# Performance work log

Measured on AMD Instinct MI355X. Metric: run time of the kernel, lower is better.

The kernel has to match this reference:

```python
import jax, jax.numpy as jnp
import numpy as np

B, DEC, ENC, H = 4, 128, 512, 768


def setup_inputs() -> dict:
    key = jax.random.key(0)
    k1, k2, k3, k4, k5 = jax.random.split(key, 5)
    scale = 1.0 / np.sqrt(H)
    return {
        "decoder_state": jax.random.normal(k1, (B, DEC, H), dtype=jnp.float32),
        "encoder_outputs": jax.random.normal(k2, (B, ENC, H), dtype=jnp.float32),
        "mask": jnp.zeros((B, DEC, ENC), dtype=jnp.float32),
        # Learned params: torch nn.Linear(H, H, bias=False) weights, stored as (in, out)
        "W1": jax.random.normal(k3, (H, H), dtype=jnp.float32) * scale,
        "W2": jax.random.normal(k4, (H, H), dtype=jnp.float32) * scale,
        "vt": jax.random.normal(k5, (H,), dtype=jnp.float32) * scale,
    }


def reference(decoder_state, encoder_outputs, mask, W1, W2, vt):
    # enc_t: (B, enc, H), dec_t: (B, dec, H)
    enc_t = jnp.einsum("beh,hk->bek", encoder_outputs, W1)
    dec_t = jnp.einsum("bdh,hk->bdk", decoder_state, W2)
    # Bahdanau additive score: tanh of broadcast sum -> (B, dec, enc, H), reduce with vt
    hidden = jnp.tanh(enc_t[:, None, :, :] + dec_t[:, :, None, :])
    log_score = jnp.einsum("bdek,k->bde", hidden, vt)
    log_score_masked = log_score + mask
    return (log_score_masked, log_score)
```

## Files before the change

### kernel.cpp

```cpp
#include <hip/hip_runtime.h>
#include <hip/hip_bf16.h>

#define B_SZ   4
#define DEC_SZ 128
#define ENC_SZ 512
#define H_SZ   768
#define OUT_N  (B_SZ * DEC_SZ * ENC_SZ)

typedef __attribute__((ext_vector_type(8))) short s8v;
typedef __attribute__((ext_vector_type(4))) float fvec4;

__device__ inline unsigned short f2bf(float x) {
  union { float f; unsigned u; } v; v.f = x;
  unsigned r = v.u + 0x7FFF + ((v.u >> 16) & 1);
  return (unsigned short)(r >> 16);
}

__device__ inline s8v load8(const unsigned short* p) { return *(const s8v*)p; }
__device__ inline s8v load8(const float* p) {
  float4 a = ((const float4*)p)[0];
  float4 b = ((const float4*)p)[1];
  unsigned short r[8] = {f2bf(a.x), f2bf(a.y), f2bf(a.z), f2bf(a.w),
                         f2bf(b.x), f2bf(b.y), f2bf(b.z), f2bf(b.w)};
  return *(const s8v*)r;
}

__global__ __launch_bounds__(256) void transpose_w(const float* __restrict__ W1,
                                                   const float* __restrict__ W2,
                                                   unsigned short* __restrict__ T1,
                                                   unsigned short* __restrict__ T2) {
  const float* W = blockIdx.z ? W2 : W1;
  unsigned short* T = blockIdx.z ? T2 : T1;
  __shared__ float tile[64][65];
  int c0 = blockIdx.x * 64;
  int r0 = blockIdx.y * 64;
  int tx = threadIdx.x & 63, ty = threadIdx.x >> 6;
#pragma unroll
  for (int i = 0; i < 16; ++i) {
    int r = ty + i * 4;
    tile[r][tx] = W[(size_t)(r0 + r) * H_SZ + c0 + tx];
  }
  __syncthreads();
#pragma unroll
  for (int i = 0; i < 16; ++i) {
    int c = ty + i * 4;
    T[(size_t)(c0 + c) * H_SZ + r0 + tx] = f2bf(tile[tx][c]);
  }
}

template <bool TILED, typename TA, typename TB>
__device__ inline void gemm_body(const TA* __restrict__ A, const TB* __restrict__ B,
                                 float* __restrict__ C, int ldc, int bx, int by) {
  const int m0 = bx * 128;
  const int n0 = by * 64;

  __shared__ unsigned short As[128][40];
  __shared__ unsigned short Bs[64][40];

  const int tid  = threadIdx.x;
  const int wave = tid >> 6;
  const int lane = tid & 63;
  const int l16  = lane & 15;
  const int quad = lane >> 4;
  const int wm   = wave * 32;

  int ar[2], ak[2];
#pragma unroll
  for (int i = 0; i < 2; ++i) {
    int seg = tid + 256 * i;
    ar[i] = seg >> 2; ak[i] = (seg & 3) * 8;
  }
  const int br = tid >> 2, bk = (tid & 3) * 8;

  fvec4 acc[2][4];
#pragma unroll
  for (int i = 0; i < 2; ++i)
#pragma unroll
    for (int j = 0; j < 4; ++j) acc[i][j] = (fvec4)0.f;

  s8v pa[2], pb;
#pragma unroll
  for (int i = 0; i < 2; ++i) pa[i] = load8(A + (size_t)(m0 + ar[i]) * H_SZ + ak[i]);
  pb = load8(B + (size_t)(n0 + br) * H_SZ + bk);

  for (int k0 = 0; k0 < H_SZ; k0 += 32) {
    __syncthreads();
#pragma unroll
    for (int i = 0; i < 2; ++i) *(s8v*)&As[ar[i]][ak[i]] = pa[i];
    *(s8v*)&Bs[br][bk] = pb;
    __syncthreads();

    if (k0 + 32 < H_SZ) {
#pragma unroll
      for (int i = 0; i < 2; ++i)
        pa[i] = load8(A + (size_t)(m0 + ar[i]) * H_SZ + k0 + 32 + ak[i]);
      pb = load8(B + (size_t)(n0 + br) * H_SZ + k0 + 32 + bk);
    }

    s8v af[2], bf[4];
#pragma unroll
    for (int i = 0; i < 2; ++i) af[i] = *(const s8v*)&As[wm + i * 16 + l16][quad * 8];
#pragma unroll
    for (int j = 0; j < 4; ++j) bf[j] = *(const s8v*)&Bs[j * 16 + l16][quad * 8];
#pragma unroll
    for (int i = 0; i < 2; ++i)
#pragma unroll
      for (int j = 0; j < 4; ++j)
        acc[i][j] = __builtin_amdgcn_mfma_f32_16x16x32_bf16(af[i], bf[j], acc[i][j], 0, 0, 0);
  }

  const float C2 = 2.885390082f;
#pragma unroll
  for (int i = 0; i < 2; ++i) {
    int mbase = m0 + wm + i * 16 + quad * 4;
#pragma unroll
    for (int j = 0; j < 4; ++j) {
      int n = n0 + j * 16 + l16;
      if (TILED) {
        float4 o;
        o.x = __builtin_amdgcn_exp2f(acc[i][j][0] * C2);
        o.y = __builtin_amdgcn_exp2f(acc[i][j][1] * C2);
        o.z = __builtin_amdgcn_exp2f(acc[i][j][2] * C2);
        o.w = __builtin_amdgcn_exp2f(acc[i][j][3] * C2);
        int bIdx = n >> 9, es = (n >> 6) & 7, el = n & 63;
        ((float4*)C)[((size_t)(bIdx * 8 + es) * 192 + (mbase >> 2)) * 64 + el] = o;
      } else {
#pragma unroll
        for (int r = 0; r < 4; ++r)
          C[(size_t)(mbase + r) * ldc + n] = __builtin_amdgcn_exp2f(acc[i][j][r] * C2);
      }
    }
  }
}

__global__ __launch_bounds__(256) void gemm_both(const unsigned short* __restrict__ W1T,
                                                 const float* __restrict__ enc,
                                                 const float* __restrict__ dec,
                                                 const unsigned short* __restrict__ W2T,
                                                 float* __restrict__ peT,
                                                 float* __restrict__ pdm) {
  int bid = blockIdx.x;
  if (bid < 192) {
    gemm_body<true>(W1T, enc, peT, 0, bid % 6, bid / 6);
  } else {
    int r = bid - 192;
    gemm_body<false>(dec, W2T, pdm, H_SZ, r % 4, r / 4);
  }
}

__device__ inline float quad_acc(float4 cur, float4 p4, float4 v4, float t) {
  float a  = fmaf(cur.x, p4.x, 1.f);
  float bq = fmaf(cur.y, p4.y, 1.f);
  float cq = fmaf(cur.z, p4.z, 1.f);
  float dq = fmaf(cur.w, p4.w, 1.f);
  float ab = a * bq, cd = cq * dq;
  float n01 = fmaf(v4.x, bq, v4.y * a);
  float n23 = fmaf(v4.z, dq, v4.w * cq);
  float num = fmaf(n23, ab, n01 * cd);
  return fmaf(num, __builtin_amdgcn_rcpf(ab * cd), t);
}

__global__ __launch_bounds__(512) void score_out(const float* __restrict__ peT,
                                                 const float* __restrict__ pdm,
                                                 const float* __restrict__ vt,
                                                 const float* __restrict__ mask,
                                                 float* __restrict__ out) {
  const int tid  = threadIdx.x;
  const int lane = tid & 63;
  const int wave = __builtin_amdgcn_readfirstlane(tid >> 6);
  const int dg   = wave & 1;
  const int kq   = wave >> 1;

  const int L    = blockIdx.x;
  const int xcd  = L & 7;
  const int slot = L >> 3;
  const int col  = xcd + 8 * (slot & 3);
  const int b    = col >> 3;
  const int es   = col & 7;
  const int d0   = (slot >> 2) * 8 + dg * 4;

  float sumv = 0.f;
#pragma unroll
  for (int j = 0; j < 12; ++j) sumv += vt[lane + 64 * j];
#pragma unroll
  for (int s = 1; s < 64; s <<= 1) sumv += __shfl_xor(sumv, s, 64);

  const float* pdr = pdm + (size_t)(b * DEC_SZ + d0) * H_SZ + kq * 192;
  const float* vth = vt + kq * 192;
  const float4* pe4 = (const float4*)peT + ((size_t)col * 192 + kq * 48) * 64 + lane;

  float t0 = 0.f, t1 = 0.f, t2 = 0.f, t3 = 0.f;
  float4 buf[8];
#pragma unroll
  for (int i = 0; i < 8; ++i) buf[i] = pe4[(size_t)i * 64];

#pragma unroll 8
  for (int c = 0; c < 48; ++c) {
    float4 cur = buf[c & 7];
    if (c + 8 < 48) buf[c & 7] = pe4[(size_t)(c + 8) * 64];
    float4 v4 = *(const float4*)(vth + c * 4);
    t0 = quad_acc(cur, *(const float4*)(pdr + c * 4), v4, t0);
    t1 = quad_acc(cur, *(const float4*)(pdr + H_SZ + c * 4), v4, t1);
    t2 = quad_acc(cur, *(const float4*)(pdr + 2 * H_SZ + c * 4), v4, t2);
    t3 = quad_acc(cur, *(const float4*)(pdr + 3 * H_SZ + c * 4), v4, t3);
  }

  __shared__ float tred[4][8][64];
  {
    int dl = dg * 4;
    tred[kq][dl + 0][lane] = t0;
    tred[kq][dl + 1][lane] = t1;
    tred[kq][dl + 2][lane] = t2;
    tred[kq][dl + 3][lane] = t3;
  }
  __syncthreads();

  if (kq == 0) {
    const int e = es * 64 + lane;
#pragma unroll
    for (int j = 0; j < 4; ++j) {
      int dl = dg * 4 + j;
      float t = tred[0][dl][lane] + tred[1][dl][lane] +
                tred[2][dl][lane] + tred[3][dl][lane];
      int d = (slot >> 2) * 8 + dl;
      size_t idx = ((size_t)(b * DEC_SZ + d)) * ENC_SZ + e;
      float s = fmaf(-2.f, t, sumv);
      out[idx] = s + mask[idx];
      out[OUT_N + idx] = s;
    }
  }
}

extern "C" void kernel_launch(void* const* d_in, const int* in_sizes, int n_in,
                              void* d_out, int out_size, void* d_ws, size_t ws_size,
                              hipStream_t stream) {
  (void)in_sizes; (void)n_in; (void)out_size; (void)ws_size;
  const float* dec  = (const float*)d_in[0];
  const float* enc  = (const float*)d_in[1];
  const float* mask = (const float*)d_in[2];
  const float* W1   = (const float*)d_in[3];
  const float* W2   = (const float*)d_in[4];
  const float* vt   = (const float*)d_in[5];
  float* out = (float*)d_out;

  float* peT = (float*)d_ws;
  float* pdm = peT + (size_t)H_SZ * B_SZ * ENC_SZ;
  unsigned short* W1T = (unsigned short*)(pdm + (size_t)B_SZ * DEC_SZ * H_SZ);
  unsigned short* W2T = W1T + (size_t)H_SZ * H_SZ;

  transpose_w<<<dim3(12, 12, 2), 256, 0, stream>>>(W1, W2, W1T, W2T);
  gemm_both<<<dim3(240), 256, 0, stream>>>(W1T, enc, dec, W2T, peT, pdm);
  score_out<<<dim3(512), 512, 0, stream>>>(peT, pdm, vt, mask, out);
}
```

Baseline: 122.8 us.

## Split score kernel K-dimension across eight waves with four decoder rows per block

The score kernel now gives each 512-thread block 4 decoder rows instead of 8. All eight waves split the hidden dimension into eighths of 96, where before there were 2 row groups times 4 quarters. The grid doubles to 1024 blocks, each wave's inner loop is half as long, and the shared-memory reduction sums 8 partials. The aim is more parallelism and shorter dependency chains per wave. The cost is that each encoder-projection tile is reused by half as many decoder rows, so its global read traffic roughly doubles.

```diff
diff --git a/kernel.cpp b/kernel.cpp
--- a/kernel.cpp
+++ b/kernel.cpp
@@ -167,9 +167,7 @@
                                                  float* __restrict__ out) {
   const int tid  = threadIdx.x;
   const int lane = tid & 63;
-  const int wave = __builtin_amdgcn_readfirstlane(tid >> 6);
-  const int dg   = wave & 1;
-  const int kq   = wave >> 1;
+  const int kq   = __builtin_amdgcn_readfirstlane(tid >> 6);
 
   const int L    = blockIdx.x;
   const int xcd  = L & 7;
@@ -177,7 +175,8 @@
   const int col  = xcd + 8 * (slot & 3);
   const int b    = col >> 3;
   const int es   = col & 7;
-  const int d0   = (slot >> 2) * 8 + dg * 4;
+  const int dblk = slot >> 2;
+  const int d0   = dblk * 4;
 
   float sumv = 0.f;
 #pragma unroll
@@ -185,9 +184,9 @@
 #pragma unroll
   for (int s = 1; s < 64; s <<= 1) sumv += __shfl_xor(sumv, s, 64);
 
-  const float* pdr = pdm + (size_t)(b * DEC_SZ + d0) * H_SZ + kq * 192;
-  const float* vth = vt + kq * 192;
-  const float4* pe4 = (const float4*)peT + ((size_t)col * 192 + kq * 48) * 64 + lane;
+  const float* pdr = pdm + (size_t)(b * DEC_SZ + d0) * H_SZ + kq * 96;
+  const float* vth = vt + kq * 96;
+  const float4* pe4 = (const float4*)peT + ((size_t)col * 192 + kq * 24) * 64 + lane;
 
   float t0 = 0.f, t1 = 0.f, t2 = 0.f, t3 = 0.f;
   float4 buf[8];
@@ -195,9 +194,9 @@
   for (int i = 0; i < 8; ++i) buf[i] = pe4[(size_t)i * 64];
 
 #pragma unroll 8
-  for (int c = 0; c < 48; ++c) {
+  for (int c = 0; c < 24; ++c) {
     float4 cur = buf[c & 7];
-    if (c + 8 < 48) buf[c & 7] = pe4[(size_t)(c + 8) * 64];
+    if (c + 8 < 24) buf[c & 7] = pe4[(size_t)(c + 8) * 64];
     float4 v4 = *(const float4*)(vth + c * 4);
     t0 = quad_acc(cur, *(const float4*)(pdr + c * 4), v4, t0);
     t1 = quad_acc(cur, *(const float4*)(pdr + H_SZ + c * 4), v4, t1);
@@ -205,29 +204,24 @@
     t3 = quad_acc(cur, *(const float4*)(pdr + 3 * H_SZ + c * 4), v4, t3);
   }
 
-  __shared__ float tred[4][8][64];
-  {
-    int dl = dg * 4;
-    tred[kq][dl + 0][lane] = t0;
-    tred[kq][dl + 1][lane] = t1;
-    tred[kq][dl + 2][lane] = t2;
-    tred[kq][dl + 3][lane] = t3;
-  }
+  __shared__ float tred[8][4][64];
+  tred[kq][0][lane] = t0;
+  tred[kq][1][lane] = t1;
+  tred[kq][2][lane] = t2;
+  tred[kq][3][lane] = t3;
   __syncthreads();
 
-  if (kq == 0) {
+  if (kq < 4) {
+    const int dl = kq;
+    float t = 0.f;
+#pragma unroll
+    for (int q = 0; q < 8; ++q) t += tred[q][dl][lane];
     const int e = es * 64 + lane;
-#pragma unroll
-    for (int j = 0; j < 4; ++j) {
-      int dl = dg * 4 + j;
-      float t = tred[0][dl][lane] + tred[1][dl][lane] +
-                tred[2][dl][lane] + tred[3][dl][lane];
-      int d = (slot >> 2) * 8 + dl;
-      size_t idx = ((size_t)(b * DEC_SZ + d)) * ENC_SZ + e;
-      float s = fmaf(-2.f, t, sumv);
-      out[idx] = s + mask[idx];
-      out[OUT_N + idx] = s;
-    }
+    int d = d0 + dl;
+    size_t idx = ((size_t)(b * DEC_SZ + d)) * ENC_SZ + e;
+    float s = fmaf(-2.f, t, sumv);
+    out[idx] = s + mask[idx];
+    out[OUT_N + idx] = s;
   }
 }
 
@@ -250,5 +244,5 @@
 
   transpose_w<<<dim3(12, 12, 2), 256, 0, stream>>>(W1, W2, W1T, W2T);
   gemm_both<<<dim3(240), 256, 0, stream>>>(W1T, enc, dec, W2T, peT, pdm);
-  score_out<<<dim3(512), 512, 0, stream>>>(peT, pdm, vt, mask, out);
-}
+  score_out<<<dim3(1024), 512, 0, stream>>>(peT, pdm, vt, mask, out);
+}
```

Result: slower. 133.3 us (+8.6%).
